# Kernel optimization log

Measured on AMD Instinct MI355X. Metric: run time of the kernel, lower is better.

The kernel has to match this reference:

```python
import jax, jax.numpy as jnp
import numpy as np

B, S, D, H, DFF = 8, 1024, 1024, 16, 4096
DK = D // H
NEG = -1000000000.0


def layernorm(x, g, b, eps=1e-5):
    mu = jnp.mean(x, axis=-1, keepdims=True)
    var = jnp.mean((x - mu) ** 2, axis=-1, keepdims=True)
    return (x - mu) / jnp.sqrt(var + eps) * g + b


def setup_inputs() -> dict:
    key = jax.random.key(0)
    ks = jax.random.split(key, 16)
    s = 0.02
    inp = {
        "x": jax.random.normal(ks[0], (B, S, D), jnp.float32),
        "binary_mask": jax.random.randint(ks[1], (B, S), 0, 2, jnp.int32),
        # per-head projections stacked: [H, D, DK]
        "Wq": jax.random.normal(ks[2], (H, D, DK), jnp.float32) * s,
        "bq": jnp.zeros((H, DK), jnp.float32),
        "Wk": jax.random.normal(ks[3], (H, D, DK), jnp.float32) * s,
        "bk": jnp.zeros((H, DK), jnp.float32),
        "Wv": jax.random.normal(ks[4], (H, D, DK), jnp.float32) * s,
        "bv": jnp.zeros((H, DK), jnp.float32),
        "Wo": jax.random.normal(ks[5], (D, D), jnp.float32) * s,
        "bo": jnp.zeros((D,), jnp.float32),
        "ga": jnp.ones((D,), jnp.float32),
        "ba": jnp.zeros((D,), jnp.float32),
        "W1": jax.random.normal(ks[6], (D, DFF), jnp.float32) * s,
        "b1": jnp.zeros((DFF,), jnp.float32),
        "W2": jax.random.normal(ks[7], (DFF, D), jnp.float32) * s,
        "b2": jnp.zeros((D,), jnp.float32),
        "gf": jnp.ones((D,), jnp.float32),
        "bf": jnp.zeros((D,), jnp.float32),
    }
    return inp


def encoder_fwd(x, binary_mask, Wq, bq, Wk, bk, Wv, bv, Wo, bo, ga, ba, W1, b1, W2, b2, gf, bf):
    # --- multi-head self-attention (heads vectorized over h axis) ---
    q = jnp.einsum("bsd,hdk->bhsk", x, Wq) + bq[None, :, None, :]
    k = jnp.einsum("bsd,hdk->bhsk", x, Wk) + bk[None, :, None, :]
    v = jnp.einsum("bsd,hdk->bhsk", x, Wv) + bv[None, :, None, :]
    score = jnp.einsum("bhik,bhjk->bhij", q, k) / jnp.sqrt(jnp.float32(DK))
    # mask: binary_mask is over KEY positions, broadcast over query dim
    score = score + jnp.where(binary_mask[:, None, None, :] == 0, NEG, 0.0)
    # NOTE: original code softmaxes over dim=1 of [B,Sq,Sk] -> the QUERY axis
    probs = jax.nn.softmax(score, axis=2)
    ctx = jnp.einsum("bhij,bhjk->bhik", probs, v)  # [B,H,S,DK]
    ctx = jnp.transpose(ctx, (0, 2, 1, 3)).reshape(x.shape[0], x.shape[1], D)
    attn_out = ctx @ Wo + bo
    y = layernorm(x + attn_out, ga, ba)
    # --- FFN ---
    h = jax.nn.relu(y @ W1 + b1)
    ffn_out = h @ W2 + b2
    return layernorm(y + ffn_out, gf, bf)


def reference(x, binary_mask, Wq, bq, Wk, bk, Wv, bv, Wo, bo, ga, ba, W1, b1, W2, b2, gf, bf):
    return encoder_fwd(x, binary_mask, Wq, bq, Wk, bk, Wv, bv, Wo, bo, ga, ba, W1, b1, W2, b2, gf, bf)
```

## Files before the change

kernel.cpp:

```cpp
#include <hip/hip_runtime.h>
#include <hip/hip_bf16.h>

typedef __bf16 bf16;
typedef __bf16 bf16x8 __attribute__((ext_vector_type(8)));
typedef __bf16 bf16x4 __attribute__((ext_vector_type(4)));
typedef float  f32x4  __attribute__((ext_vector_type(4)));

#define NB 8
#define NS 1024
#define ND 1024
#define NH 16
#define NDK 64
#define NDFF 4096

static __device__ __forceinline__ f32x4 mfma16(bf16x8 a, bf16x8 b, f32x4 c) {
    return __builtin_amdgcn_mfma_f32_16x16x32_bf16(a, b, c, 0, 0, 0);
}

#define GLDS(g, l) __builtin_amdgcn_global_load_lds( \
    (const __attribute__((address_space(1))) void*)(g), \
    (__attribute__((address_space(3))) void*)(l), 16, 0, 0)

__global__ __launch_bounds__(256) void cvt_x(const float* __restrict__ in,
                                             bf16* __restrict__ out, int n4)
// ... 58 lines not shown
    int type = n >> 10, hk = n & 1023;
    const float* bb = (type == 0) ? bq : (type == 1 ? bk : bv);
    float v = bb[hk];
    if (type == 0) v *= 0.125f;
    bqkv[n] = v;
}

__device__ __forceinline__ void gemm_bt_core(
    const bf16* __restrict__ A, const bf16* __restrict__ BT, int K,
    int rowBase, int colBase, f32x4 (&acc)[4][4], bf16* As, bf16* Bs)
{
    const int tid = threadIdx.x;
    const int lane = tid & 63, wid = tid >> 6;
    const int wr = (wid >> 1) * 64, wc = (wid & 1) * 64;
    const int lrow = lane & 15, lq = lane >> 4;
    const int srow = wid * 32 + (lane >> 3);
    const int gblk = (lane & 7) ^ ((lane >> 3) & 7);
    const bf16* Arow = A + (size_t)(rowBase + srow) * K + gblk * 8;
    const bf16* Brow = BT + (size_t)(colBase + srow) * K + gblk * 8;
    const int co0 = ((lq) ^ (lrow & 7)) * 8;
    const int co1 = ((4 + lq) ^ (lrow & 7)) * 8;
    f32x4 zz = {0.f, 0.f, 0.f, 0.f};
    #pragma unroll
    for (int i = 0; i < 4; i++)
        #pragma unroll
        for (int j = 0; j < 4; j++) acc[i][j] = zz;
    for (int k0 = 0; k0 < K; k0 += 64) {
        __syncthreads();
        #pragma unroll
        for (int it = 0; it < 4; it++)
            GLDS(Arow + (size_t)it * 8 * K + k0, As + (wid * 32 + it * 8) * 64);
        #pragma unroll
        for (int it = 0; it < 4; it++)
            GLDS(Brow + (size_t)it * 8 * K + k0, Bs + (wid * 32 + it * 8) * 64);
        __syncthreads();
        #pragma unroll
        for (int kh = 0; kh < 2; kh++) {
            const int co = kh ? co1 : co0;
            bf16x8 af[4], bfr[4];
            #pragma unroll
            for (int tt = 0; tt < 4; tt++) {
                af[tt]  = *(const bf16x8*)&As[(wr + tt * 16 + lrow) * 64 + co];
                bfr[tt] = *(const bf16x8*)&Bs[(wc + tt * 16 + lrow) * 64 + co];
            }
            #pragma unroll
            for (int i = 0; i < 4; i++)
                #pragma unroll
                for (int j = 0; j < 4; j++)
                    acc[i][j] = mfma16(af[i], bfr[j], acc[i][j]);
        }
    }
}

__global__ __launch_bounds__(256) void g1_qkv(
    const bf16* __restrict__ x, const bf16* __restrict__ wqkvT, const float* __restrict__ bqkv,
    bf16* __restrict__ Q, bf16* __restrict__ Kb, bf16* __restrict__ Vb)
{
    __shared__ bf16 As[128 * 64], Bs[128 * 64];
    f32x4 acc[4][4];
    int rowBase = blockIdx.x * 128, colBase = blockIdx.y * 128;
    gemm_bt_core(x, wqkvT, ND, rowBase, colBase, acc, As, Bs);
    const int tid = threadIdx.x, lane = tid & 63, wid = tid >> 6;
    const int wr = (wid >> 1) * 64, wc = (wid & 1) * 64, lrow = lane & 15, lq = lane >> 4;
    #pragma unroll
    for (int j = 0; j < 4; j++) {
        int gcol = colBase + wc + j * 16 + lrow;
        float bias = bqkv[gcol];
        int type = gcol >> 10, h = (gcol >> 6) & 15, kk = gcol & 63;
        bf16* dst = (type == 0) ? Q : (type == 1 ? Kb : Vb);
        #pragma unroll
        for (int i = 0; i < 4; i++) {
            #pragma unroll
            for (int r = 0; r < 4; r++) {
                int grow = rowBase + wr + i * 16 + lq * 4 + r;
                int b = grow >> 10, s = grow & 1023;
                dst[((size_t)(b * NH + h) * NS + s) * NDK + kk] = (bf16)(acc[i][j][r] + bias);
            }
        }
    }
}

__global__ __launch_bounds__(256) void vt_trans(
    const bf16* __restrict__ Vb, bf16* __restrict__ Vt)
{
    __shared__ bf16 T[64 * 72];
    int bh = blockIdx.y, s0 = blockIdx.x * 64;
    const bf16* src = Vb + ((size_t)bh * NS + s0) * NDK;
    int tid = threadIdx.x;
    #pragma unroll
    for (int it = 0; it < 2; it++) {
        int g = tid + it * 256;
        int row = g >> 3, c = (g & 7) * 8;
        *(bf16x8*)&T[row * 72 + c] = *(const bf16x8*)&src[row * NDK + c];
    }
    __syncthreads();
    #pragma unroll
    for (int it = 0; it < 2; it++) {
        int g = tid + it * 256;
        int kk = g >> 3, sc = (g & 7) * 8;
        bf16x8 v;
        #pragma unroll
        for (int t = 0; t < 8; t++) v[t] = T[(sc + t) * 72 + kk];
        *(bf16x8*)&Vt[((size_t)bh * NDK + kk) * NS + s0 + sc] = v;
    }
}

__global__ __launch_bounds__(256) void g2_stats(
    const bf16* __restrict__ Q, const bf16* __restrict__ Kb,
    const int* __restrict__ mask, float2* __restrict__ alpha)
{
    __shared__ bf16 Qs[128 * 64];
    int bh = blockIdx.y, b = bh >> 4;
    int jBase = blockIdx.x * 128;
    const bf16* Kp = Kb + (size_t)bh * NS * NDK;
    const bf16* Qp = Q + (size_t)bh * NS * NDK;
    const int tid = threadIdx.x, lane = tid & 63, wid = tid >> 6;
    const int lrow = lane & 15, lq = lane >> 4;
    bf16x8 kf[2][2];
    #pragma unroll
    for (int jt = 0; jt < 2; jt++)
        #pragma unroll
        for (int kh = 0; kh < 2; kh++)
            kf[jt][kh] = *(const bf16x8*)&Kp[(size_t)(jBase + wid * 32 + jt * 16 + lrow) * NDK + kh * 32 + lq * 8];
    const int srow = lane >> 3;
    const int gblk = (lane & 7) ^ srow;
    float Lacc[2][4];
    #pragma unroll
    for (int jt = 0; jt < 2; jt++)
        #pragma unroll
        for (int r = 0; r < 4; r++) Lacc[jt][r] = 0.f;
    f32x4 zz = {0.f, 0.f, 0.f, 0.f};
    for (int i0 = 0; i0 < NS; i0 += 128) {
        __syncthreads();
        #pragma unroll
        for (int it = 0; it < 4; it++)
            GLDS(Qp + (size_t)(i0 + wid * 32 + it * 8 + srow) * NDK + gblk * 8,
                 Qs + (wid * 32 + it * 8) * 64);
        __syncthreads();
        #pragma unroll
        for (int it = 0; it < 8; it++) {
            bf16x8 qb[2];
            #pragma unroll
            for (int kh = 0; kh < 2; kh++)
                qb[kh] = *(const bf16x8*)&Qs[(it * 16 + lrow) * 64 + ((kh * 4 + lq) ^ (lrow & 7)) * 8];
            #pragma unroll
            for (int jt = 0; jt < 2; jt++) {
                f32x4 s = mfma16(kf[jt][0], qb[0], zz);
                s = mfma16(kf[jt][1], qb[1], s);
                #pragma unroll
                for (int r = 0; r < 4; r++) Lacc[jt][r] += __expf(s[r]);
            }
        }
    }
    #pragma unroll
    for (int jt = 0; jt < 2; jt++) {
        #pragma unroll
        for (int r = 0; r < 4; r++) {
            float v = Lacc[jt][r];
            v += __shfl_xor(v, 1); v += __shfl_xor(v, 2);
            v += __shfl_xor(v, 4); v += __shfl_xor(v, 8);
            if (lrow == 0) {
                int j = jBase + wid * 32 + jt * 16 + lq * 4 + r;
                int m = mask[b * NS + j];
                float2 ac;
                ac.x = m ? 1.f / v : 0.f;
                ac.y = m ? 0.f : (1.f / 1024.f);
                alpha[(size_t)bh * NS + j] = ac;
            }
        }
    }
}

__global__ __launch_bounds__(256) void g3_ctx(
    const bf16* __restrict__ Q, const bf16* __restrict__ Kb, const bf16* __restrict__ Vt,
    const float2* __restrict__ alpha, bf16* __restrict__ ctx)
{
    __shared__ bf16 Ks[64 * 64];
    __shared__ bf16 Vs[64 * 64];
    __shared__ bf16 Ps[4 * 64 * 64];
    int bh = blockIdx.y, iBase = blockIdx.x * 256;
    int b = bh >> 4, h = bh & 15;
    const bf16* Qp = Q + (size_t)bh * NS * NDK;
    const bf16* Kp = Kb + (size_t)bh * NS * NDK;
    const bf16* Vp = Vt + (size_t)bh * NDK * NS;
    const float2* al = alpha + (size_t)bh * NS;
    const int tid = threadIdx.x, lane = tid & 63, wid = tid >> 6;
    const int lrow = lane & 15, lq = lane >> 4;
    const int iw = iBase + wid * 64;
    bf16x8 qf[4][2];
    #pragma unroll
    for (int it = 0; it < 4; it++)
        #pragma unroll
        for (int kh = 0; kh < 2; kh++)
            qf[it][kh] = *(const bf16x8*)&Qp[(size_t)(iw + it * 16 + lrow) * NDK + kh * 32 + lq * 8];
    const int srow = lane >> 3;
    const int gblk = (lane & 7) ^ srow;
    f32x4 cacc[4][4];
    f32x4 zz = {0.f, 0.f, 0.f, 0.f};
    #pragma unroll
    for (int it = 0; it < 4; it++)
        #pragma unroll
        for (int kt = 0; kt < 4; kt++) cacc[it][kt] = zz;
    bf16* Pw = Ps + wid * 64 * 64;
    for (int j0 = 0; j0 < NS; j0 += 64) {
        __syncthreads();
        #pragma unroll
        for (int it = 0; it < 2; it++)
            GLDS(Kp + (size_t)(j0 + wid * 16 + it * 8 + srow) * NDK + gblk * 8,
                 Ks + (wid * 16 + it * 8) * 64);
        #pragma unroll
        for (int it = 0; it < 2; it++)
            GLDS(Vp + (size_t)(wid * 16 + it * 8 + srow) * NS + j0 + gblk * 8,
                 Vs + (wid * 16 + it * 8) * 64);
        __syncthreads();
        bf16x8 kb[4][2];
        #pragma unroll
        for (int jt = 0; jt < 4; jt++)
            #pragma unroll
            for (int kh = 0; kh < 2; kh++)
                kb[jt][kh] = *(const bf16x8*)&Ks[(jt * 16 + lrow) * 64 + ((kh * 4 + lq) ^ (lrow & 7)) * 8];
        #pragma unroll
        for (int jt = 0; jt < 4; jt++) {
            float2 acj[4];
            #pragma unroll
            for (int r = 0; r < 4; r++) acj[r] = al[j0 + jt * 16 + lq * 4 + r];
            #pragma unroll
            for (int it = 0; it < 4; it++) {
                f32x4 s = mfma16(kb[jt][0], qf[it][0], zz);
                s = mfma16(kb[jt][1], qf[it][1], s);
                bf16x4 pv;
                #pragma unroll
                for (int r = 0; r < 4; r++)
                    pv[r] = (bf16)(acj[r].x * __expf(s[r]) + acj[r].y);
                int i = it * 16 + lrow;
                int jb = jt * 2 + (lq >> 1);
                *(bf16x4*)&Pw[i * 64 + ((jb ^ (i & 7)) * 8) + (lq & 1) * 4] = pv;
            }
        }
        bf16x8 vb[4][2];
        #pragma unroll
        for (int kt = 0; kt < 4; kt++)
            #pragma unroll
            for (int kh = 0; kh < 2; kh++)
                vb[kt][kh] = *(const bf16x8*)&Vs[(kt * 16 + lrow) * 64 + ((kh * 4 + lq) ^ (lrow & 7)) * 8];
        #pragma unroll
        for (int it = 0; it < 4; it++) {
            bf16x8 pa[2];
            #pragma unroll
            for (int kh = 0; kh < 2; kh++)
                pa[kh] = *(const bf16x8*)&Pw[(it * 16 + lrow) * 64 + ((kh * 4 + lq) ^ (lrow & 7)) * 8];
            #pragma unroll
            for (int kt = 0; kt < 4; kt++) {
                cacc[it][kt] = mfma16(pa[0], vb[kt][0], cacc[it][kt]);
                cacc[it][kt] = mfma16(pa[1], vb[kt][1], cacc[it][kt]);
            }
        }
    }
    #pragma unroll
    for (int kt = 0; kt < 4; kt++) {
        int col = h * NDK + kt * 16 + lrow;
        #pragma unroll
        for (int it = 0; it < 4; it++) {
            #pragma unroll
            for (int r = 0; r < 4; r++) {
                int i = iw + it * 16 + lq * 4 + r;
                ctx[(size_t)(b * NS + i) * ND + col] = (bf16)cacc[it][kt][r];
            }
        }
    }
}

__global__ __launch_bounds__(256) void g4_proj(
    const bf16* __restrict__ ctx, const bf16* __restrict__ WoT, const float* __restrict__ bo,
    const bf16* __restrict__ xb, bf16* __restrict__ t1b)
{
    __shared__ bf16 As[128 * 64], Bs[128 * 64];
    f32x4 acc[4][4];
    int rowBase = blockIdx.x * 128, colBase = blockIdx.y * 128;
    gemm_bt_core(ctx, WoT, ND, rowBase, colBase, acc, As, Bs);
    const int tid = threadIdx.x, lane = tid & 63, wid = tid >> 6;
    const int wr = (wid >> 1) * 64, wc = (wid & 1) * 64, lrow = lane & 15, lq = lane >> 4;
    #pragma unroll
    for (int j = 0; j < 4; j++) {
        int gcol = colBase + wc + j * 16 + lrow;
        float bias = bo[gcol];
        #pragma unroll
        for (int i = 0; i < 4; i++) {
            #pragma unroll
            for (int r = 0; r < 4; r++) {
                int grow = rowBase + wr + i * 16 + lq * 4 + r;
                float v = acc[i][j][r] + bias + (float)xb[(size_t)grow * ND + gcol];
                t1b[(size_t)grow * ND + gcol] = (bf16)v;
            }
        }
    }
}

__device__ __forceinline__ void gemmA_core(
    const bf16* __restrict__ A, const bf16* __restrict__ BT, int K,
    int rowBase, int colBase, f32x4 (&acc)[8][4], bf16* As, bf16* Bs)
{
    constexpr int ABUF = 256 * 64, BBUF = 256 * 64;
    const int tid = threadIdx.x, lane = tid & 63, wid = tid >> 6;
    const int wm = wid >> 2, wn = wid & 3;
    const int lrow = lane & 15, lq = lane >> 4;
    const int srow = lane >> 3, gblk = (lane & 7) ^ srow;
    const int co0 = (lq ^ (lrow & 7)) * 8;
    const int co1 = ((4 + lq) ^ (lrow & 7)) * 8;
    f32x4 zz = {0.f, 0.f, 0.f, 0.f};
    #pragma unroll
    for (int i = 0; i < 8; i++)
        #pragma unroll
        for (int j = 0; j < 4; j++) acc[i][j] = zz;
    const bf16* Ag = A  + (size_t)(rowBase + wid * 8 + srow) * K + gblk * 8;
    const bf16* Bg = BT + (size_t)(colBase + wid * 8 + srow) * K + gblk * 8;

#define SGA(kt, bi, rr) GLDS(Ag + (size_t)(kt) * 64 + (size_t)(rr) * 64 * K, \
                             As + (bi) * ABUF + ((rr) * 64 + wid * 8) * 64)
#define SGB(kt, bi, rr) GLDS(Bg + (size_t)(kt) * 64 + (size_t)(rr) * 64 * K, \
                             Bs + (bi) * BBUF + ((rr) * 64 + wid * 8) * 64)
#define RDA(MS) do { _Pragma("unroll") for (int i_ = 0; i_ < 4; i_++) { \
    int ro_ = (wm * 128 + (MS) * 64 + i_ * 16 + lrow) * 64; \
    af[i_][0] = *(const bf16x8*)&Ab[ro_ + co0]; \
    af[i_][1] = *(const bf16x8*)&Ab[ro_ + co1]; } } while (0)
#define RDB(dst, NS_) do { _Pragma("unroll") for (int j_ = 0; j_ < 2; j_++) { \
    int ro_ = (wn * 64 + (NS_) * 32 + j_ * 16 + lrow) * 64; \
    dst[j_][0] = *(const bf16x8*)&Bb[ro_ + co0]; \
    dst[j_][1] = *(const bf16x8*)&Bb[ro_ + co1]; } } while (0)
#define CLUSTER_A(bfx, IO, JO) do { \
    __builtin_amdgcn_s_barrier(); \
    asm volatile("s_waitcnt lgkmcnt(0)" ::: "memory"); \
    __builtin_amdgcn_sched_barrier(0); \
    __builtin_amdgcn_s_setprio(1); \
    _Pragma("unroll") \
    for (int i_ = 0; i_ < 4; i_++) \
        _Pragma("unroll") \
        for (int j_ = 0; j_ < 2; j_++) { \
            acc[(IO) + i_][(JO) + j_] = mfma16(af[i_][0], bfx[j_][0], acc[(IO) + i_][(JO) + j_]); \
            acc[(IO) + i_][(JO) + j_] = mfma16(af[i_][1], bfx[j_][1], acc[(IO) + i_][(JO) + j_]); \
        } \
    __builtin_amdgcn_s_setprio(0); \
} while (0)

    const int nt = K >> 6;
    SGA(0, 0, 0); SGA(0, 0, 2);
    SGB(0, 0, 0); SGB(0, 0, 1); SGB(0, 0, 2); SGB(0, 0, 3);
    SGA(0, 0, 1); SGA(0, 0, 3);
    asm volatile("s_waitcnt vmcnt(2)" ::: "memory");
    __builtin_amdgcn_s_barrier();

    int cur = 0;
    for (int t = 0; t < nt; ++t, cur ^= 1) {
        const bf16* Ab = As + cur * ABUF;
        const bf16* Bb = Bs + cur * BBUF;
        const bool pf = (t + 1 < nt);
        bf16x8 af[4][2], bf0[2][2], bf1[2][2];
        RDA(0); RDB(bf0, 0);
        if (pf) { SGA(t + 1, cur ^ 1, 0); SGA(t + 1, cur ^ 1, 2); }
        CLUSTER_A(bf0, 0, 0);
        __builtin_amdgcn_s_barrier();
        RDB(bf1, 1);
        if (pf) { SGB(t + 1, cur ^ 1, 0); SGB(t + 1, cur ^ 1, 1); }
        CLUSTER_A(bf1, 0, 2);
        if (pf) asm volatile("s_waitcnt vmcnt(4)" ::: "memory");
        else    asm volatile("s_waitcnt vmcnt(0)" ::: "memory");
        __builtin_amdgcn_s_barrier();
        RDA(1);
        if (pf) { SGB(t + 1, cur ^ 1, 2); SGB(t + 1, cur ^ 1, 3); }
        CLUSTER_A(bf1, 4, 2);
        __builtin_amdgcn_s_barrier();
        RDB(bf0, 0);
        if (pf) { SGA(t + 1, cur ^ 1, 1); SGA(t + 1, cur ^ 1, 3); }
        CLUSTER_A(bf0, 4, 0);
        if (pf) asm volatile("s_waitcnt vmcnt(2)" ::: "memory");
        __builtin_amdgcn_s_barrier();
    }
#undef SGA
#undef SGB
#undef RDA
#undef RDB
#undef CLUSTER_A
}

__device__ __forceinline__ void gemmB_core(
    const bf16* __restrict__ A, const bf16* __restrict__ BT, int K,
    int rowBase, int colBase, f32x4 (&acc)[4][4], bf16* As, bf16* Bs)
{
    constexpr int ABUF = 128 * 64, BBUF = 256 * 64;
    const int tid = threadIdx.x, lane = tid & 63, wid = tid >> 6;
    const int wm = wid >> 2, wn = wid & 3;
    const int lrow = lane & 15, lq = lane >> 4;
    const int srow = lane >> 3, gblk = (lane & 7) ^ srow;
    const int co0 = (lq ^ (lrow & 7)) * 8;
    const int co1 = ((4 + lq) ^ (lrow & 7)) * 8;
    f32x4 zz = {0.f, 0.f, 0.f, 0.f};
    #pragma unroll
    for (int i = 0; i < 4; i++)
        #pragma unroll
        for (int j = 0; j < 4; j++) acc[i][j] = zz;
    const bf16* Ag = A  + (size_t)(rowBase + wid * 8 + srow) * K + gblk * 8;
    const bf16* Bg = BT + (size_t)(colBase + wid * 8 + srow) * K + gblk * 8;

#define SGA2(kt, bi, rr) GLDS(Ag + (size_t)(kt) * 64 + (size_t)(rr) * 64 * K, \
                              As + (bi) * ABUF + ((rr) * 64 + wid * 8) * 64)
#define SGB2(kt, bi, rr) GLDS(Bg + (size_t)(kt) * 64 + (size_t)(rr) * 64 * K, \
                              Bs + (bi) * BBUF + ((rr) * 64 + wid * 8) * 64)
#define RDA2() do { _Pragma("unroll") for (int i_ = 0; i_ < 4; i_++) { \
    int ro_ = (wm * 64 + i_ * 16 + lrow) * 64; \
    af[i_][0] = *(const bf16x8*)&Ab[ro_ + co0]; \
    af[i_][1] = *(const bf16x8*)&Ab[ro_ + co1]; } } while (0)
#define RDB2(dst, NS_) do { _Pragma("unroll") for (int j_ = 0; j_ < 2; j_++) { \
    int ro_ = (wn * 64 + (NS_) * 32 + j_ * 16 + lrow) * 64; \
    dst[j_][0] = *(const bf16x8*)&Bb[ro_ + co0]; \
    dst[j_][1] = *(const bf16x8*)&Bb[ro_ + co1]; } } while (0)
#define CLUSTER_B(bfx, JO) do { \
    __builtin_amdgcn_s_barrier(); \
    asm volatile("s_waitcnt lgkmcnt(0)" ::: "memory"); \
    __builtin_amdgcn_sched_barrier(0); \
    __builtin_amdgcn_s_setprio(1); \
    _Pragma("unroll") \
    for (int i_ = 0; i_ < 4; i_++) \
        _Pragma("unroll") \
        for (int j_ = 0; j_ < 2; j_++) { \
            acc[i_][(JO) + j_] = mfma16(af[i_][0], bfx[j_][0], acc[i_][(JO) + j_]); \
            acc[i_][(JO) + j_] = mfma16(af[i_][1], bfx[j_][1], acc[i_][(JO) + j_]); \
        } \
    __builtin_amdgcn_s_setprio(0); \
} while (0)

    const int nt = K >> 6;
    SGA2(0, 0, 0); SGA2(0, 0, 1);
    SGB2(0, 0, 0); SGB2(0, 0, 1); SGB2(0, 0, 2); SGB2(0, 0, 3);
    SGA2(1, 1, 0); SGA2(1, 1, 1);
    SGB2(1, 1, 0); SGB2(1, 1, 1); SGB2(1, 1, 2); SGB2(1, 1, 3);
    asm volatile("s_waitcnt vmcnt(6)" ::: "memory");
    __builtin_amdgcn_s_barrier();

    int ci = 0, si = 2;
    for (int t = 0; t < nt; ++t) {
        const bf16* Ab = As + ci * ABUF;
        const bf16* Bb = Bs + ci * BBUF;
        const bool pf = (t + 2 < nt);
        bf16x8 af[4][2], bf0[2][2], bf1[2][2];
        RDA2(); RDB2(bf0, 0);
        if (pf) { SGA2(t + 2, si, 0); SGA2(t + 2, si, 1); SGB2(t + 2, si, 0); SGB2(t + 2, si, 1); }
        CLUSTER_B(bf0, 0);
        __builtin_amdgcn_s_barrier();
        RDB2(bf1, 1);
        if (pf) { SGB2(t + 2, si, 2); SGB2(t + 2, si, 3); }
        CLUSTER_B(bf1, 2);
        if (pf)                asm volatile("s_waitcnt vmcnt(6)" ::: "memory");
        else if (t + 1 < nt)   asm volatile("s_waitcnt vmcnt(0)" ::: "memory");
        __builtin_amdgcn_s_barrier();
        ci = (ci == 2) ? 0 : ci + 1;
        si = (si == 2) ? 0 : si + 1;
    }
#undef SGA2
#undef SGB2
#undef RDA2
#undef RDB2
#undef CLUSTER_B
}

__global__ __launch_bounds__(512, 2) void g5_ffn1(
    const bf16* __restrict__ y, const bf16* __restrict__ W1T, const float* __restrict__ b1,
    bf16* __restrict__ hb)
{
    __shared__ bf16 As[2 * 256 * 64], Bs[2 * 256 * 64];
    f32x4 acc[8][4];
    int g = blockIdx.x;
    int sw = (g & 7) * 64 + (g >> 3);
    int bm = sw >> 4, bn = sw & 15;
    int rowBase = bm * 256, colBase = bn * 256;
    gemmA_core(y, W1T, ND, rowBase, colBase, acc, As, Bs);
    const int tid = threadIdx.x, lane = tid & 63, wid = tid >> 6;
    const int wm = wid >> 2, wn = wid & 3, lrow = lane & 15, lq = lane >> 4;
    #pragma unroll
    for (int j = 0; j < 4; j++) {
        int gcol = colBase + wn * 64 + j * 16 + lrow;
        float bias = b1[gcol];
        #pragma unroll
        for (int i = 0; i < 8; i++) {
            #pragma unroll
            for (int r = 0; r < 4; r++) {
                int grow = rowBase + wm * 128 + i * 16 + lq * 4 + r;
                float v = fmaxf(acc[i][j][r] + bias, 0.f);
                hb[(size_t)grow * NDFF + gcol] = (bf16)v;
            }
        }
    }
}

__global__ __launch_bounds__(512, 2) void g6_ffn2(
    const bf16* __restrict__ hb, const bf16* __restrict__ W2T, const float* __restrict__ b2,
    const bf16* __restrict__ yb, bf16* __restrict__ zb)
{
    __shared__ bf16 As[3 * 128 * 64], Bs[3 * 256 * 64];
    f32x4 acc[4][4];
    int g = blockIdx.x;
    int sw = (g & 7) * 32 + (g >> 3);
    int bm = sw >> 2, bn = sw & 3;
    int rowBase = bm * 128, colBase = bn * 256;
    gemmB_core(hb, W2T, NDFF, rowBase, colBase, acc, As, Bs);
    const int tid = threadIdx.x, lane = tid & 63, wid = tid >> 6;
    const int wm = wid >> 2, wn = wid & 3, lrow = lane & 15, lq = lane >> 4;
    #pragma unroll
    for (int j = 0; j < 4; j++) {
        int gcol = colBase + wn * 64 + j * 16 + lrow;
        float bias = b2[gcol];
        #pragma unroll
        for (int i = 0; i < 4; i++) {
            #pragma unroll
            for (int r = 0; r < 4; r++) {
                int grow = rowBase + wm * 64 + i * 16 + lq * 4 + r;
                float v = acc[i][j][r] + bias + (float)yb[(size_t)grow * ND + gcol];
                zb[(size_t)grow * ND + gcol] = (bf16)v;
            }
        }
    }
}

__global__ __launch_bounds__(256) void ln_kernel(
    const bf16* __restrict__ in, bf16* __restrict__ outb, float* __restrict__ outf,
    const float* __restrict__ g, const float* __restrict__ bb)
{
    int row = blockIdx.x, tid = threadIdx.x;
    const bf16* p = in + (size_t)row * ND;
// ... 21 lines not shown
        ((float*)&of)[k] = yv;
        ob[k] = (bf16)yv;
    }
    if (outb) *(bf16x4*)&outb[(size_t)row * ND + tid * 4] = ob;
    if (outf) ((float4*)(outf + (size_t)row * ND))[tid] = of;
}

extern "C" void kernel_launch(void* const* d_in, const int* in_sizes, int n_in,
                              void* d_out, int out_size, void* d_ws, size_t ws_size,
                              hipStream_t stream)
{
    const float* x    = (const float*)d_in[0];
    const int*   mask = (const int*)d_in[1];
    const float* Wq   = (const float*)d_in[2];
    const float* bq   = (const float*)d_in[3];
    const float* Wk   = (const float*)d_in[4];
    const float* bk   = (const float*)d_in[5];
    const float* Wv   = (const float*)d_in[6];
    const float* bv   = (const float*)d_in[7];
    const float* Wo   = (const float*)d_in[8];
    const float* bo   = (const float*)d_in[9];
    const float* ga   = (const float*)d_in[10];
    const float* ba   = (const float*)d_in[11];
    const float* W1   = (const float*)d_in[12];
    const float* b1   = (const float*)d_in[13];
    const float* W2   = (const float*)d_in[14];
    const float* b2   = (const float*)d_in[15];
    const float* gf   = (const float*)d_in[16];
    const float* bfb  = (const float*)d_in[17];

    size_t off = 0;
    auto alloc = [&](size_t n) { char* p = (char*)d_ws + off; off += (n + 255) & ~(size_t)255; return (void*)p; };
    bf16*   wqkvT = (bf16*)  alloc((size_t)3072 * 1024 * 2);
    bf16*   WoT   = (bf16*)  alloc((size_t)1024 * 1024 * 2);
    bf16*   W1T   = (bf16*)  alloc((size_t)4096 * 1024 * 2);
    bf16*   W2T   = (bf16*)  alloc((size_t)1024 * 4096 * 2);
    float*  bqkv  = (float*) alloc(3072 * 4);
    float2* alpha = (float2*)alloc((size_t)NB * NH * NS * 8);
    bf16*   xb    = (bf16*)  alloc((size_t)8192 * 1024 * 2);
    bf16*   ub    = (bf16*)  alloc((size_t)8192 * 4096 * 2);
    bf16*   Qb    = ub;
    bf16*   Kb    = ub + (size_t)8192 * 1024;
    bf16*   Vt    = ub + (size_t)2 * 8192 * 1024;
    bf16*   ctx   = ub + (size_t)3 * 8192 * 1024;
    bf16*   hb    = ub;
    bf16*   t1b   = (bf16*)  alloc((size_t)8192 * 1024 * 2);
    bf16*   Vb    = t1b;
    bf16*   zb    = t1b;
    bf16*   yb    = (bf16*)  alloc((size_t)8192 * 1024 * 2);

    cvt_x<<<8192, 256, 0, stream>>>(x, xb, 8192 * 1024 / 4);
    prep_transpose<<<3072, 256, 0, stream>>>(Wq, Wk, Wv, Wo, W1, W2, wqkvT, WoT, W1T, W2T);
    prep_bias<<<12, 256, 0, stream>>>(bq, bk, bv, bqkv);
    g1_qkv<<<dim3(64, 24), 256, 0, stream>>>(xb, wqkvT, bqkv, Qb, Kb, Vb);
    vt_trans<<<dim3(16, 128), 256, 0, stream>>>(Vb, Vt);
    g2_stats<<<dim3(8, 128), 256, 0, stream>>>(Qb, Kb, mask, alpha);
    g3_ctx<<<dim3(4, 128), 256, 0, stream>>>(Qb, Kb, Vt, alpha, ctx);
    g4_proj<<<dim3(64, 8), 256, 0, stream>>>(ctx, WoT, bo, xb, t1b);
    ln_kernel<<<8192, 256, 0, stream>>>(t1b, yb, nullptr, ga, ba);
    g5_ffn1<<<512, 512, 0, stream>>>(yb, W1T, b1, hb);
    g6_ffn2<<<256, 512, 0, stream>>>(hb, W2T, b2, yb, zb);
    ln_kernel<<<8192, 256, 0, stream>>>(zb, nullptr, (float*)d_out, gf, bfb);
}
```

Baseline: 501.7 us.

## Rewrite 256x256 GEMM pipeline and move QKV projection onto it

Replaces the FFN1 GEMM core with a new 8-phase pipeline that double-buffers A and B tiles, staging the next k-tile while MFMA clusters run on the current one under explicit barriers and vmcnt waits. The QKV projection moves from a 128x128 tile kernel with 256 threads to the 512-thread 256x256 tile path, which gives more data reuse per block and fewer blocks. The remaining attention and projection kernels are only moved within the file. The tighter barrier schedule and larger tiles may reduce occupancy, and the QKV grid of 384 blocks may not fill the GPU evenly.

```diff
diff --git a/kernel.cpp b/kernel.cpp
--- a/kernel.cpp
+++ b/kernel.cpp
@@ -134,259 +134,15 @@
     }
 }
 
-__global__ __launch_bounds__(256) void g1_qkv(
-    const bf16* __restrict__ x, const bf16* __restrict__ wqkvT, const float* __restrict__ bqkv,
-    bf16* __restrict__ Q, bf16* __restrict__ Kb, bf16* __restrict__ Vb)
-{
-    __shared__ bf16 As[128 * 64], Bs[128 * 64];
-    f32x4 acc[4][4];
-    int rowBase = blockIdx.x * 128, colBase = blockIdx.y * 128;
-    gemm_bt_core(x, wqkvT, ND, rowBase, colBase, acc, As, Bs);
-    const int tid = threadIdx.x, lane = tid & 63, wid = tid >> 6;
-    const int wr = (wid >> 1) * 64, wc = (wid & 1) * 64, lrow = lane & 15, lq = lane >> 4;
-    #pragma unroll
-    for (int j = 0; j < 4; j++) {
-        int gcol = colBase + wc + j * 16 + lrow;
-        float bias = bqkv[gcol];
-        int type = gcol >> 10, h = (gcol >> 6) & 15, kk = gcol & 63;
-        bf16* dst = (type == 0) ? Q : (type == 1 ? Kb : Vb);
-        #pragma unroll
-        for (int i = 0; i < 4; i++) {
-            #pragma unroll
-            for (int r = 0; r < 4; r++) {
-                int grow = rowBase + wr + i * 16 + lq * 4 + r;
-                int b = grow >> 10, s = grow & 1023;
-                dst[((size_t)(b * NH + h) * NS + s) * NDK + kk] = (bf16)(acc[i][j][r] + bias);
-            }
-        }
-    }
-}
-
-__global__ __launch_bounds__(256) void vt_trans(
-    const bf16* __restrict__ Vb, bf16* __restrict__ Vt)
-{
-    __shared__ bf16 T[64 * 72];
-    int bh = blockIdx.y, s0 = blockIdx.x * 64;
-    const bf16* src = Vb + ((size_t)bh * NS + s0) * NDK;
-    int tid = threadIdx.x;
-    #pragma unroll
-    for (int it = 0; it < 2; it++) {
-        int g = tid + it * 256;
-        int row = g >> 3, c = (g & 7) * 8;
-        *(bf16x8*)&T[row * 72 + c] = *(const bf16x8*)&src[row * NDK + c];
-    }
-    __syncthreads();
-    #pragma unroll
-    for (int it = 0; it < 2; it++) {
-        int g = tid + it * 256;
-        int kk = g >> 3, sc = (g & 7) * 8;
-        bf16x8 v;
-        #pragma unroll
-        for (int t = 0; t < 8; t++) v[t] = T[(sc + t) * 72 + kk];
-        *(bf16x8*)&Vt[((size_t)bh * NDK + kk) * NS + s0 + sc] = v;
-    }
-}
-
-__global__ __launch_bounds__(256) void g2_stats(
-    const bf16* __restrict__ Q, const bf16* __restrict__ Kb,
-    const int* __restrict__ mask, float2* __restrict__ alpha)
-{
-    __shared__ bf16 Qs[128 * 64];
-    int bh = blockIdx.y, b = bh >> 4;
-    int jBase = blockIdx.x * 128;
-    const bf16* Kp = Kb + (size_t)bh * NS * NDK;
-    const bf16* Qp = Q + (size_t)bh * NS * NDK;
-    const int tid = threadIdx.x, lane = tid & 63, wid = tid >> 6;
-    const int lrow = lane & 15, lq = lane >> 4;
-    bf16x8 kf[2][2];
-    #pragma unroll
-    for (int jt = 0; jt < 2; jt++)
-        #pragma unroll
-        for (int kh = 0; kh < 2; kh++)
-            kf[jt][kh] = *(const bf16x8*)&Kp[(size_t)(jBase + wid * 32 + jt * 16 + lrow) * NDK + kh * 32 + lq * 8];
-    const int srow = lane >> 3;
-    const int gblk = (lane & 7) ^ srow;
-    float Lacc[2][4];
-    #pragma unroll
-    for (int jt = 0; jt < 2; jt++)
-        #pragma unroll
-        for (int r = 0; r < 4; r++) Lacc[jt][r] = 0.f;
-    f32x4 zz = {0.f, 0.f, 0.f, 0.f};
-    for (int i0 = 0; i0 < NS; i0 += 128) {
-        __syncthreads();
-        #pragma unroll
-        for (int it = 0; it < 4; it++)
-            GLDS(Qp + (size_t)(i0 + wid * 32 + it * 8 + srow) * NDK + gblk * 8,
-                 Qs + (wid * 32 + it * 8) * 64);
-        __syncthreads();
-        #pragma unroll
-        for (int it = 0; it < 8; it++) {
-            bf16x8 qb[2];
-            #pragma unroll
-            for (int kh = 0; kh < 2; kh++)
-                qb[kh] = *(const bf16x8*)&Qs[(it * 16 + lrow) * 64 + ((kh * 4 + lq) ^ (lrow & 7)) * 8];
-            #pragma unroll
-            for (int jt = 0; jt < 2; jt++) {
-                f32x4 s = mfma16(kf[jt][0], qb[0], zz);
-                s = mfma16(kf[jt][1], qb[1], s);
-                #pragma unroll
-                for (int r = 0; r < 4; r++) Lacc[jt][r] += __expf(s[r]);
-            }
-        }
-    }
-    #pragma unroll
-    for (int jt = 0; jt < 2; jt++) {
-        #pragma unroll
-        for (int r = 0; r < 4; r++) {
-            float v = Lacc[jt][r];
-            v += __shfl_xor(v, 1); v += __shfl_xor(v, 2);
-            v += __shfl_xor(v, 4); v += __shfl_xor(v, 8);
-            if (lrow == 0) {
-                int j = jBase + wid * 32 + jt * 16 + lq * 4 + r;
-                int m = mask[b * NS + j];
-                float2 ac;
-                ac.x = m ? 1.f / v : 0.f;
-                ac.y = m ? 0.f : (1.f / 1024.f);
-                alpha[(size_t)bh * NS + j] = ac;
-            }
-        }
-    }
-}
-
-__global__ __launch_bounds__(256) void g3_ctx(
-    const bf16* __restrict__ Q, const bf16* __restrict__ Kb, const bf16* __restrict__ Vt,
-    const float2* __restrict__ alpha, bf16* __restrict__ ctx)
-{
-    __shared__ bf16 Ks[64 * 64];
-    __shared__ bf16 Vs[64 * 64];
-    __shared__ bf16 Ps[4 * 64 * 64];
-    int bh = blockIdx.y, iBase = blockIdx.x * 256;
-    int b = bh >> 4, h = bh & 15;
-    const bf16* Qp = Q + (size_t)bh * NS * NDK;
-    const bf16* Kp = Kb + (size_t)bh * NS * NDK;
-    const bf16* Vp = Vt + (size_t)bh * NDK * NS;
-    const float2* al = alpha + (size_t)bh * NS;
-    const int tid = threadIdx.x, lane = tid & 63, wid = tid >> 6;
-    const int lrow = lane & 15, lq = lane >> 4;
-    const int iw = iBase + wid * 64;
-    bf16x8 qf[4][2];
-    #pragma unroll
-    for (int it = 0; it < 4; it++)
-        #pragma unroll
-        for (int kh = 0; kh < 2; kh++)
-            qf[it][kh] = *(const bf16x8*)&Qp[(size_t)(iw + it * 16 + lrow) * NDK + kh * 32 + lq * 8];
-    const int srow = lane >> 3;
-    const int gblk = (lane & 7) ^ srow;
-    f32x4 cacc[4][4];
-    f32x4 zz = {0.f, 0.f, 0.f, 0.f};
-    #pragma unroll
-    for (int it = 0; it < 4; it++)
-        #pragma unroll
-        for (int kt = 0; kt < 4; kt++) cacc[it][kt] = zz;
-    bf16* Pw = Ps + wid * 64 * 64;
-    for (int j0 = 0; j0 < NS; j0 += 64) {
-        __syncthreads();
-        #pragma unroll
-        for (int it = 0; it < 2; it++)
-            GLDS(Kp + (size_t)(j0 + wid * 16 + it * 8 + srow) * NDK + gblk * 8,
-                 Ks + (wid * 16 + it * 8) * 64);
-        #pragma unroll
-        for (int it = 0; it < 2; it++)
-            GLDS(Vp + (size_t)(wid * 16 + it * 8 + srow) * NS + j0 + gblk * 8,
-                 Vs + (wid * 16 + it * 8) * 64);
-        __syncthreads();
-        bf16x8 kb[4][2];
-        #pragma unroll
-        for (int jt = 0; jt < 4; jt++)
-            #pragma unroll
-            for (int kh = 0; kh < 2; kh++)
-                kb[jt][kh] = *(const bf16x8*)&Ks[(jt * 16 + lrow) * 64 + ((kh * 4 + lq) ^ (lrow & 7)) * 8];
-        #pragma unroll
-        for (int jt = 0; jt < 4; jt++) {
-            float2 acj[4];
-            #pragma unroll
-            for (int r = 0; r < 4; r++) acj[r] = al[j0 + jt * 16 + lq * 4 + r];
-            #pragma unroll
-            for (int it = 0; it < 4; it++) {
-                f32x4 s = mfma16(kb[jt][0], qf[it][0], zz);
-                s = mfma16(kb[jt][1], qf[it][1], s);
-                bf16x4 pv;
-                #pragma unroll
-                for (int r = 0; r < 4; r++)
-                    pv[r] = (bf16)(acj[r].x * __expf(s[r]) + acj[r].y);
-                int i = it * 16 + lrow;
-                int jb = jt * 2 + (lq >> 1);
-                *(bf16x4*)&Pw[i * 64 + ((jb ^ (i & 7)) * 8) + (lq & 1) * 4] = pv;
-            }
-        }
-        bf16x8 vb[4][2];
-        #pragma unroll
-        for (int kt = 0; kt < 4; kt++)
-            #pragma unroll
-            for (int kh = 0; kh < 2; kh++)
-                vb[kt][kh] = *(const bf16x8*)&Vs[(kt * 16 + lrow) * 64 + ((kh * 4 + lq) ^ (lrow & 7)) * 8];
-        #pragma unroll
-        for (int it = 0; it < 4; it++) {
-            bf16x8 pa[2];
-            #pragma unroll
-            for (int kh = 0; kh < 2; kh++)
-                pa[kh] = *(const bf16x8*)&Pw[(it * 16 + lrow) * 64 + ((kh * 4 + lq) ^ (lrow & 7)) * 8];
-            #pragma unroll
-            for (int kt = 0; kt < 4; kt++) {
-                cacc[it][kt] = mfma16(pa[0], vb[kt][0], cacc[it][kt]);
-                cacc[it][kt] = mfma16(pa[1], vb[kt][1], cacc[it][kt]);
-            }
-        }
-    }
-    #pragma unroll
-    for (int kt = 0; kt < 4; kt++) {
-        int col = h * NDK + kt * 16 + lrow;
-        #pragma unroll
-        for (int it = 0; it < 4; it++) {
-            #pragma unroll
-            for (int r = 0; r < 4; r++) {
-                int i = iw + it * 16 + lq * 4 + r;
-                ctx[(size_t)(b * NS + i) * ND + col] = (bf16)cacc[it][kt][r];
-            }
-        }
-    }
-}
-
-__global__ __launch_bounds__(256) void g4_proj(
-    const bf16* __restrict__ ctx, const bf16* __restrict__ WoT, const float* __restrict__ bo,
-    const bf16* __restrict__ xb, bf16* __restrict__ t1b)
-{
-    __shared__ bf16 As[128 * 64], Bs[128 * 64];
-    f32x4 acc[4][4];
-    int rowBase = blockIdx.x * 128, colBase = blockIdx.y * 128;
-    gemm_bt_core(ctx, WoT, ND, rowBase, colBase, acc, As, Bs);
-    const int tid = threadIdx.x, lane = tid & 63, wid = tid >> 6;
-    const int wr = (wid >> 1) * 64, wc = (wid & 1) * 64, lrow = lane & 15, lq = lane >> 4;
-    #pragma unroll
-    for (int j = 0; j < 4; j++) {
-        int gcol = colBase + wc + j * 16 + lrow;
-        float bias = bo[gcol];
-        #pragma unroll
-        for (int i = 0; i < 4; i++) {
-            #pragma unroll
-            for (int r = 0; r < 4; r++) {
-                int grow = rowBase + wr + i * 16 + lq * 4 + r;
-                float v = acc[i][j][r] + bias + (float)xb[(size_t)grow * ND + gcol];
-                t1b[(size_t)grow * ND + gcol] = (bf16)v;
-            }
-        }
-    }
-}
-
-__device__ __forceinline__ void gemmA_core(
+__device__ __forceinline__ void gemm8p(
     const bf16* __restrict__ A, const bf16* __restrict__ BT, int K,
     int rowBase, int colBase, f32x4 (&acc)[8][4], bf16* As, bf16* Bs)
 {
-    constexpr int ABUF = 256 * 64, BBUF = 256 * 64;
+    constexpr int SETSZ = 256 * 64;
     const int tid = threadIdx.x, lane = tid & 63, wid = tid >> 6;
     const int wm = wid >> 2, wn = wid & 3;
     const int lrow = lane & 15, lq = lane >> 4;
-    const int srow = lane >> 3, gblk = (lane & 7) ^ srow;
+    const int s8 = lane >> 3, gblk = (lane & 7) ^ s8;
     const int co0 = (lq ^ (lrow & 7)) * 8;
     const int co1 = ((4 + lq) ^ (lrow & 7)) * 8;
     f32x4 zz = {0.f, 0.f, 0.f, 0.f};
@@ -394,74 +150,89 @@
     for (int i = 0; i < 8; i++)
         #pragma unroll
         for (int j = 0; j < 4; j++) acc[i][j] = zz;
-    const bf16* Ag = A  + (size_t)(rowBase + wid * 8 + srow) * K + gblk * 8;
-    const bf16* Bg = BT + (size_t)(colBase + wid * 8 + srow) * K + gblk * 8;
-
-#define SGA(kt, bi, rr) GLDS(Ag + (size_t)(kt) * 64 + (size_t)(rr) * 64 * K, \
-                             As + (bi) * ABUF + ((rr) * 64 + wid * 8) * 64)
-#define SGB(kt, bi, rr) GLDS(Bg + (size_t)(kt) * 64 + (size_t)(rr) * 64 * K, \
-                             Bs + (bi) * BBUF + ((rr) * 64 + wid * 8) * 64)
-#define RDA(MS) do { _Pragma("unroll") for (int i_ = 0; i_ < 4; i_++) { \
-    int ro_ = (wm * 128 + (MS) * 64 + i_ * 16 + lrow) * 64; \
-    af[i_][0] = *(const bf16x8*)&Ab[ro_ + co0]; \
-    af[i_][1] = *(const bf16x8*)&Ab[ro_ + co1]; } } while (0)
-#define RDB(dst, NS_) do { _Pragma("unroll") for (int j_ = 0; j_ < 2; j_++) { \
-    int ro_ = (wn * 64 + (NS_) * 32 + j_ * 16 + lrow) * 64; \
-    dst[j_][0] = *(const bf16x8*)&Bb[ro_ + co0]; \
-    dst[j_][1] = *(const bf16x8*)&Bb[ro_ + co1]; } } while (0)
-#define CLUSTER_A(bfx, IO, JO) do { \
-    __builtin_amdgcn_s_barrier(); \
-    asm volatile("s_waitcnt lgkmcnt(0)" ::: "memory"); \
-    __builtin_amdgcn_sched_barrier(0); \
+    const bf16* Ag = A  + (size_t)(rowBase + wid * 8 + s8) * K + gblk * 8;
+    const bf16* Bg = BT + (size_t)(colBase + wid * 8 + s8) * K + gblk * 8;
+
+#define SG_A(kt, set, h) do { \
+    GLDS(Ag + (size_t)((h) * 128) * K + (kt) * 64, \
+         As + (set) * SETSZ + ((h) * 128 + wid * 8) * 64); \
+    GLDS(Ag + (size_t)((h) * 128 + 64) * K + (kt) * 64, \
+         As + (set) * SETSZ + ((h) * 128 + 64 + wid * 8) * 64); \
+} while (0)
+#define SG_B(kt, set, h) do { \
+    GLDS(Bg + (size_t)((h) * 128) * K + (kt) * 64, \
+         Bs + (set) * SETSZ + ((h) * 128 + wid * 8) * 64); \
+    GLDS(Bg + (size_t)((h) * 128 + 64) * K + (kt) * 64, \
+         Bs + (set) * SETSZ + ((h) * 128 + 64 + wid * 8) * 64); \
+} while (0)
+#define RD_A(dst, base, ms) do { _Pragma("unroll") for (int i_ = 0; i_ < 4; i_++) { \
+    int ro_ = (wm * 128 + (ms) * 64 + i_ * 16 + lrow) * 64; \
+    dst[i_][0] = *(const bf16x8*)&(base)[ro_ + co0]; \
+    dst[i_][1] = *(const bf16x8*)&(base)[ro_ + co1]; } } while (0)
+#define RD_B(dst, base, ns) do { _Pragma("unroll") for (int j_ = 0; j_ < 2; j_++) { \
+    int ro_ = (wn * 64 + (ns) * 32 + j_ * 16 + lrow) * 64; \
+    dst[j_][0] = *(const bf16x8*)&(base)[ro_ + co0]; \
+    dst[j_][1] = *(const bf16x8*)&(base)[ro_ + co1]; } } while (0)
+#define CL8(av, bv, ms, ns) do { \
     __builtin_amdgcn_s_setprio(1); \
-    _Pragma("unroll") \
-    for (int i_ = 0; i_ < 4; i_++) \
-        _Pragma("unroll") \
-        for (int j_ = 0; j_ < 2; j_++) { \
-            acc[(IO) + i_][(JO) + j_] = mfma16(af[i_][0], bfx[j_][0], acc[(IO) + i_][(JO) + j_]); \
-            acc[(IO) + i_][(JO) + j_] = mfma16(af[i_][1], bfx[j_][1], acc[(IO) + i_][(JO) + j_]); \
-        } \
+    _Pragma("unroll") for (int i_ = 0; i_ < 4; i_++) \
+    _Pragma("unroll") for (int j_ = 0; j_ < 2; j_++) { \
+        acc[(ms) * 4 + i_][(ns) * 2 + j_] = \
+            mfma16(av[i_][0], bv[j_][0], acc[(ms) * 4 + i_][(ns) * 2 + j_]); \
+        acc[(ms) * 4 + i_][(ns) * 2 + j_] = \
+            mfma16(av[i_][1], bv[j_][1], acc[(ms) * 4 + i_][(ns) * 2 + j_]); } \
     __builtin_amdgcn_s_setprio(0); \
 } while (0)
-
-    const int nt = K >> 6;
-    SGA(0, 0, 0); SGA(0, 0, 2);
-    SGB(0, 0, 0); SGB(0, 0, 1); SGB(0, 0, 2); SGB(0, 0, 3);
-    SGA(0, 0, 1); SGA(0, 0, 3);
-    asm volatile("s_waitcnt vmcnt(2)" ::: "memory");
-    __builtin_amdgcn_s_barrier();
-
-    int cur = 0;
-    for (int t = 0; t < nt; ++t, cur ^= 1) {
-        const bf16* Ab = As + cur * ABUF;
-        const bf16* Bb = Bs + cur * BBUF;
-        const bool pf = (t + 1 < nt);
-        bf16x8 af[4][2], bf0[2][2], bf1[2][2];
-        RDA(0); RDB(bf0, 0);
-        if (pf) { SGA(t + 1, cur ^ 1, 0); SGA(t + 1, cur ^ 1, 2); }
-        CLUSTER_A(bf0, 0, 0);
-        __builtin_amdgcn_s_barrier();
-        RDB(bf1, 1);
-        if (pf) { SGB(t + 1, cur ^ 1, 0); SGB(t + 1, cur ^ 1, 1); }
-        CLUSTER_A(bf1, 0, 2);
-        if (pf) asm volatile("s_waitcnt vmcnt(4)" ::: "memory");
-        else    asm volatile("s_waitcnt vmcnt(0)" ::: "memory");
-        __builtin_amdgcn_s_barrier();
-        RDA(1);
-        if (pf) { SGB(t + 1, cur ^ 1, 2); SGB(t + 1, cur ^ 1, 3); }
-        CLUSTER_A(bf1, 4, 2);
-        __builtin_amdgcn_s_barrier();
-        RDB(bf0, 0);
-        if (pf) { SGA(t + 1, cur ^ 1, 1); SGA(t + 1, cur ^ 1, 3); }
-        CLUSTER_A(bf0, 4, 0);
-        if (pf) asm volatile("s_waitcnt vmcnt(2)" ::: "memory");
-        __builtin_amdgcn_s_barrier();
-    }
-#undef SGA
-#undef SGB
-#undef RDA
-#undef RDB
-#undef CLUSTER_A
+#define BAR8 __builtin_amdgcn_s_barrier()
+#define VM4 asm volatile("s_waitcnt vmcnt(4)" ::: "memory")
+#define VM0 asm volatile("s_waitcnt vmcnt(0)" ::: "memory")
+
+    const int nt = K >> 6, nIter = nt >> 1;
+    SG_B(0, 0, 0); SG_B(0, 0, 1);
+    SG_A(0, 0, 0); SG_A(0, 0, 1);
+    SG_B(1, 1, 0); SG_B(1, 1, 1);
+    VM4; BAR8;
+    const bf16* A0b = As;           const bf16* B0b = Bs;
+    const bf16* A1b = As + SETSZ;   const bf16* B1b = Bs + SETSZ;
+    for (int J = 0; J < nIter; ++J) {
+        const int v = 2 * J + 1;
+        const bool pf = (J + 1 < nIter);
+        bf16x8 a0[4][2], a1[4][2], b0[2][2], b1[2][2];
+        RD_A(a0, A0b, 0); RD_B(b0, B0b, 0);
+        SG_A(v, 1, 0);
+        BAR8; CL8(a0, b0, 0, 0); BAR8;
+        RD_B(b1, B0b, 1);
+        SG_A(v, 1, 1);
+        BAR8; CL8(a0, b1, 0, 1); BAR8;
+        RD_A(a1, A0b, 1);
+        if (pf) SG_B(v + 1, 0, 0);
+        BAR8; CL8(a1, b1, 1, 1); BAR8;
+        if (pf) SG_B(v + 1, 0, 1);
+        BAR8; CL8(a1, b0, 1, 0);
+        if (pf) { VM4; } else { VM0; }
+        BAR8;
+        RD_A(a0, A1b, 0); RD_B(b0, B1b, 0);
+        if (pf) SG_A(v + 1, 0, 0);
+        BAR8; CL8(a0, b0, 0, 0); BAR8;
+        RD_B(b1, B1b, 1);
+        if (pf) SG_A(v + 1, 0, 1);
+        BAR8; CL8(a0, b1, 0, 1); BAR8;
+        RD_A(a1, A1b, 1);
+        if (pf) SG_B(v + 2, 1, 0);
+        BAR8; CL8(a1, b1, 1, 1); BAR8;
+        if (pf) SG_B(v + 2, 1, 1);
+        BAR8; CL8(a1, b0, 1, 0);
+        if (pf) { VM4; } else { VM0; }
+        BAR8;
+    }
+#undef SG_A
+#undef SG_B
+#undef RD_A
+#undef RD_B
+#undef CL8
+#undef BAR8
+#undef VM4
+#undef VM0
 }
 
 __device__ __forceinline__ void gemmB_core(
@@ -544,6 +315,253 @@
 #undef CLUSTER_B
 }
 
+__global__ __launch_bounds__(512, 2) void g1_qkv(
+    const bf16* __restrict__ x, const bf16* __restrict__ wqkvT, const float* __restrict__ bqkv,
+    bf16* __restrict__ Q, bf16* __restrict__ Kb, bf16* __restrict__ Vb)
+{
+    __shared__ bf16 As[2 * 256 * 64], Bs[2 * 256 * 64];
+    f32x4 acc[8][4];
+    int g = blockIdx.x;
+    int sw = (g & 7) * 48 + (g >> 3);
+    int bm = sw / 12, bn = sw % 12;
+    int rowBase = bm * 256, colBase = bn * 256;
+    gemm8p(x, wqkvT, ND, rowBase, colBase, acc, As, Bs);
+    const int tid = threadIdx.x, lane = tid & 63, wid = tid >> 6;
+    const int wm = wid >> 2, wn = wid & 3, lrow = lane & 15, lq = lane >> 4;
+    #pragma unroll
+    for (int j = 0; j < 4; j++) {
+        int gcol = colBase + wn * 64 + j * 16 + lrow;
+        float bias = bqkv[gcol];
+        int type = gcol >> 10, h = (gcol >> 6) & 15, kk = gcol & 63;
+        bf16* dst = (type == 0) ? Q : (type == 1 ? Kb : Vb);
+        #pragma unroll
+        for (int i = 0; i < 8; i++) {
+            #pragma unroll
+            for (int r = 0; r < 4; r++) {
+                int grow = rowBase + wm * 128 + i * 16 + lq * 4 + r;
+                int b = grow >> 10, s = grow & 1023;
+                dst[((size_t)(b * NH + h) * NS + s) * NDK + kk] = (bf16)(acc[i][j][r] + bias);
+            }
+        }
+    }
+}
+
+__global__ __launch_bounds__(256) void vt_trans(
+    const bf16* __restrict__ Vb, bf16* __restrict__ Vt)
+{
+    __shared__ bf16 T[64 * 72];
+    int bh = blockIdx.y, s0 = blockIdx.x * 64;
+    const bf16* src = Vb + ((size_t)bh * NS + s0) * NDK;
+    int tid = threadIdx.x;
+    #pragma unroll
+    for (int it = 0; it < 2; it++) {
+        int g = tid + it * 256;
+        int row = g >> 3, c = (g & 7) * 8;
+        *(bf16x8*)&T[row * 72 + c] = *(const bf16x8*)&src[row * NDK + c];
+    }
+    __syncthreads();
+    #pragma unroll
+    for (int it = 0; it < 2; it++) {
+        int g = tid + it * 256;
+        int kk = g >> 3, sc = (g & 7) * 8;
+        bf16x8 v;
+        #pragma unroll
+        for (int t = 0; t < 8; t++) v[t] = T[(sc + t) * 72 + kk];
+        *(bf16x8*)&Vt[((size_t)bh * NDK + kk) * NS + s0 + sc] = v;
+    }
+}
+
+__global__ __launch_bounds__(256) void g2_stats(
+    const bf16* __restrict__ Q, const bf16* __restrict__ Kb,
+    const int* __restrict__ mask, float2* __restrict__ alpha)
+{
+    __shared__ bf16 Qs[128 * 64];
+    int bh = blockIdx.y, b = bh >> 4;
+    int jBase = blockIdx.x * 128;
+    const bf16* Kp = Kb + (size_t)bh * NS * NDK;
+    const bf16* Qp = Q + (size_t)bh * NS * NDK;
+    const int tid = threadIdx.x, lane = tid & 63, wid = tid >> 6;
+    const int lrow = lane & 15, lq = lane >> 4;
+    bf16x8 kf[2][2];
+    #pragma unroll
+    for (int jt = 0; jt < 2; jt++)
+        #pragma unroll
+        for (int kh = 0; kh < 2; kh++)
+            kf[jt][kh] = *(const bf16x8*)&Kp[(size_t)(jBase + wid * 32 + jt * 16 + lrow) * NDK + kh * 32 + lq * 8];
+    const int srow = lane >> 3;
+    const int gblk = (lane & 7) ^ srow;
+    float Lacc[2][4];
+    #pragma unroll
+    for (int jt = 0; jt < 2; jt++)
+        #pragma unroll
+        for (int r = 0; r < 4; r++) Lacc[jt][r] = 0.f;
+    f32x4 zz = {0.f, 0.f, 0.f, 0.f};
+    for (int i0 = 0; i0 < NS; i0 += 128) {
+        __syncthreads();
+        #pragma unroll
+        for (int it = 0; it < 4; it++)
+            GLDS(Qp + (size_t)(i0 + wid * 32 + it * 8 + srow) * NDK + gblk * 8,
+                 Qs + (wid * 32 + it * 8) * 64);
+        __syncthreads();
+        #pragma unroll
+        for (int it = 0; it < 8; it++) {
+            bf16x8 qb[2];
+            #pragma unroll
+            for (int kh = 0; kh < 2; kh++)
+                qb[kh] = *(const bf16x8*)&Qs[(it * 16 + lrow) * 64 + ((kh * 4 + lq) ^ (lrow & 7)) * 8];
+            #pragma unroll
+            for (int jt = 0; jt < 2; jt++) {
+                f32x4 s = mfma16(kf[jt][0], qb[0], zz);
+                s = mfma16(kf[jt][1], qb[1], s);
+                #pragma unroll
+                for (int r = 0; r < 4; r++) Lacc[jt][r] += __expf(s[r]);
+            }
+        }
+    }
+    #pragma unroll
+    for (int jt = 0; jt < 2; jt++) {
+        #pragma unroll
+        for (int r = 0; r < 4; r++) {
+            float v = Lacc[jt][r];
+            v += __shfl_xor(v, 1); v += __shfl_xor(v, 2);
+            v += __shfl_xor(v, 4); v += __shfl_xor(v, 8);
+            if (lrow == 0) {
+                int j = jBase + wid * 32 + jt * 16 + lq * 4 + r;
+                int m = mask[b * NS + j];
+                float2 ac;
+                ac.x = m ? 1.f / v : 0.f;
+                ac.y = m ? 0.f : (1.f / 1024.f);
+                alpha[(size_t)bh * NS + j] = ac;
+            }
+        }
+    }
+}
+
+__global__ __launch_bounds__(256) void g3_ctx(
+    const bf16* __restrict__ Q, const bf16* __restrict__ Kb, const bf16* __restrict__ Vt,
+    const float2* __restrict__ alpha, bf16* __restrict__ ctx)
+{
+    __shared__ bf16 Ks[64 * 64];
+    __shared__ bf16 Vs[64 * 64];
+    __shared__ bf16 Ps[4 * 64 * 64];
+    int bh = blockIdx.y, iBase = blockIdx.x * 256;
+    int b = bh >> 4, h = bh & 15;
+    const bf16* Qp = Q + (size_t)bh * NS * NDK;
+    const bf16* Kp = Kb + (size_t)bh * NS * NDK;
+    const bf16* Vp = Vt + (size_t)bh * NDK * NS;
+    const float2* al = alpha + (size_t)bh * NS;
+    const int tid = threadIdx.x, lane = tid & 63, wid = tid >> 6;
+    const int lrow = lane & 15, lq = lane >> 4;
+    const int iw = iBase + wid * 64;
+    bf16x8 qf[4][2];
+    #pragma unroll
+    for (int it = 0; it < 4; it++)
+        #pragma unroll
+        for (int kh = 0; kh < 2; kh++)
+            qf[it][kh] = *(const bf16x8*)&Qp[(size_t)(iw + it * 16 + lrow) * NDK + kh * 32 + lq * 8];
+    const int srow = lane >> 3;
+    const int gblk = (lane & 7) ^ srow;
+    f32x4 cacc[4][4];
+    f32x4 zz = {0.f, 0.f, 0.f, 0.f};
+    #pragma unroll
+    for (int it = 0; it < 4; it++)
+        #pragma unroll
+        for (int kt = 0; kt < 4; kt++) cacc[it][kt] = zz;
+    bf16* Pw = Ps + wid * 64 * 64;
+    for (int j0 = 0; j0 < NS; j0 += 64) {
+        __syncthreads();
+        #pragma unroll
+        for (int it = 0; it < 2; it++)
+            GLDS(Kp + (size_t)(j0 + wid * 16 + it * 8 + srow) * NDK + gblk * 8,
+                 Ks + (wid * 16 + it * 8) * 64);
+        #pragma unroll
+        for (int it = 0; it < 2; it++)
+            GLDS(Vp + (size_t)(wid * 16 + it * 8 + srow) * NS + j0 + gblk * 8,
+                 Vs + (wid * 16 + it * 8) * 64);
+        __syncthreads();
+        bf16x8 kb[4][2];
+        #pragma unroll
+        for (int jt = 0; jt < 4; jt++)
+            #pragma unroll
+            for (int kh = 0; kh < 2; kh++)
+                kb[jt][kh] = *(const bf16x8*)&Ks[(jt * 16 + lrow) * 64 + ((kh * 4 + lq) ^ (lrow & 7)) * 8];
+        #pragma unroll
+        for (int jt = 0; jt < 4; jt++) {
+            float2 acj[4];
+            #pragma unroll
+            for (int r = 0; r < 4; r++) acj[r] = al[j0 + jt * 16 + lq * 4 + r];
+            #pragma unroll
+            for (int it = 0; it < 4; it++) {
+                f32x4 s = mfma16(kb[jt][0], qf[it][0], zz);
+                s = mfma16(kb[jt][1], qf[it][1], s);
+                bf16x4 pv;
+                #pragma unroll
+                for (int r = 0; r < 4; r++)
+                    pv[r] = (bf16)(acj[r].x * __expf(s[r]) + acj[r].y);
+                int i = it * 16 + lrow;
+                int jb = jt * 2 + (lq >> 1);
+                *(bf16x4*)&Pw[i * 64 + ((jb ^ (i & 7)) * 8) + (lq & 1) * 4] = pv;
+            }
+        }
+        bf16x8 vb[4][2];
+        #pragma unroll
+        for (int kt = 0; kt < 4; kt++)
+            #pragma unroll
+            for (int kh = 0; kh < 2; kh++)
+                vb[kt][kh] = *(const bf16x8*)&Vs[(kt * 16 + lrow) * 64 + ((kh * 4 + lq) ^ (lrow & 7)) * 8];
+        #pragma unroll
+        for (int it = 0; it < 4; it++) {
+            bf16x8 pa[2];
+            #pragma unroll
+            for (int kh = 0; kh < 2; kh++)
+                pa[kh] = *(const bf16x8*)&Pw[(it * 16 + lrow) * 64 + ((kh * 4 + lq) ^ (lrow & 7)) * 8];
+            #pragma unroll
+            for (int kt = 0; kt < 4; kt++) {
+                cacc[it][kt] = mfma16(pa[0], vb[kt][0], cacc[it][kt]);
+                cacc[it][kt] = mfma16(pa[1], vb[kt][1], cacc[it][kt]);
+            }
+        }
+    }
+    #pragma unroll
+    for (int kt = 0; kt < 4; kt++) {
+        int col = h * NDK + kt * 16 + lrow;
+        #pragma unroll
+        for (int it = 0; it < 4; it++) {
+            #pragma unroll
+            for (int r = 0; r < 4; r++) {
+                int i = iw + it * 16 + lq * 4 + r;
+                ctx[(size_t)(b * NS + i) * ND + col] = (bf16)cacc[it][kt][r];
+            }
+        }
+    }
+}
+
+__global__ __launch_bounds__(256) void g4_proj(
+    const bf16* __restrict__ ctx, const bf16* __restrict__ WoT, const float* __restrict__ bo,
+    const bf16* __restrict__ xb, bf16* __restrict__ t1b)
+{
+    __shared__ bf16 As[128 * 64], Bs[128 * 64];
+    f32x4 acc[4][4];
+    int rowBase = blockIdx.x * 128, colBase = blockIdx.y * 128;
+    gemm_bt_core(ctx, WoT, ND, rowBase, colBase, acc, As, Bs);
+    const int tid = threadIdx.x, lane = tid & 63, wid = tid >> 6;
+    const int wr = (wid >> 1) * 64, wc = (wid & 1) * 64, lrow = lane & 15, lq = lane >> 4;
+    #pragma unroll
+    for (int j = 0; j < 4; j++) {
+        int gcol = colBase + wc + j * 16 + lrow;
+        float bias = bo[gcol];
+        #pragma unroll
+        for (int i = 0; i < 4; i++) {
+            #pragma unroll
+            for (int r = 0; r < 4; r++) {
+                int grow = rowBase + wr + i * 16 + lq * 4 + r;
+                float v = acc[i][j][r] + bias + (float)xb[(size_t)grow * ND + gcol];
+                t1b[(size_t)grow * ND + gcol] = (bf16)v;
+            }
+        }
+    }
+}
+
 __global__ __launch_bounds__(512, 2) void g5_ffn1(
     const bf16* __restrict__ y, const bf16* __restrict__ W1T, const float* __restrict__ b1,
     bf16* __restrict__ hb)
@@ -554,7 +572,7 @@
     int sw = (g & 7) * 64 + (g >> 3);
     int bm = sw >> 4, bn = sw & 15;
     int rowBase = bm * 256, colBase = bn * 256;
-    gemmA_core(y, W1T, ND, rowBase, colBase, acc, As, Bs);
+    gemm8p(y, W1T, ND, rowBase, colBase, acc, As, Bs);
     const int tid = threadIdx.x, lane = tid & 63, wid = tid >> 6;
     const int wm = wid >> 2, wn = wid & 3, lrow = lane & 15, lq = lane >> 4;
     #pragma unroll
@@ -682,7 +700,7 @@
     cvt_x<<<8192, 256, 0, stream>>>(x, xb, 8192 * 1024 / 4);
     prep_transpose<<<3072, 256, 0, stream>>>(Wq, Wk, Wv, Wo, W1, W2, wqkvT, WoT, W1T, W2T);
     prep_bias<<<12, 256, 0, stream>>>(bq, bk, bv, bqkv);
-    g1_qkv<<<dim3(64, 24), 256, 0, stream>>>(xb, wqkvT, bqkv, Qb, Kb, Vb);
+    g1_qkv<<<384, 512, 0, stream>>>(xb, wqkvT, bqkv, Qb, Kb, Vb);
     vt_trans<<<dim3(16, 128), 256, 0, stream>>>(Vb, Vt);
     g2_stats<<<dim3(8, 128), 256, 0, stream>>>(Qb, Kb, mask, alpha);
     g3_ctx<<<dim3(4, 128), 256, 0, stream>>>(Qb, Kb, Vt, alpha, ctx);
```

New measurement: 517.6 us. 3.2% more time.
